# Optimization experiments

Hardware: AMD Instinct MI355X
Metric: run time of the kernel (lower is better)

The kernel has to match this reference:

```python
import jax, jax.numpy as jnp
import numpy as np

B, U, C, M = 4096, 1024, 5000, 20

def setup_inputs() -> dict:
    key = jax.random.key(0)
    ks = jax.random.split(key, 9)
    inputs = jax.random.randint(ks[0], (B, 1), 0, C).astype(jnp.int32)
    states = 0.1 * jax.random.normal(ks[1], (B, U + 2), dtype=jnp.float32)
    bias_z = jnp.zeros((U,), jnp.float32)
    recurrent_kernel = 0.02 * jax.random.normal(ks[2], (U, 4 * U), dtype=jnp.float32)
    kernel_c = 0.02 * jax.random.normal(ks[3], (C, 4 * U), dtype=jnp.float32)
    bias = jnp.zeros((3 * U,), jnp.float32)
    kernel_d = 0.1 * jax.random.normal(ks[4], (2, 4 * U), dtype=jnp.float32)
    Wgmm_part1 = 0.05 * jax.random.normal(ks[5], (U, 3 * M), dtype=jnp.float32)
    bgmm_part1 = jnp.zeros((3 * M,), jnp.float32)
    return {"inputs": inputs, "states": states, "bias_z": bias_z,
            "recurrent_kernel": recurrent_kernel, "kernel_c": kernel_c,
            "bias": bias, "kernel_d": kernel_d,
            "Wgmm_part1": Wgmm_part1, "bgmm_part1": bgmm_part1}

def exp_safe(x):
    return jnp.clip(jnp.exp(x), 1e-10, 1e10)

def reference(inputs, states, bias_z, recurrent_kernel, kernel_c, bias,
              kernel_d, Wgmm_part1, bgmm_part1):
    u = bias_z.shape[0]
    h_tm1 = states[:, :-2]          # [B, U]
    _d = states[:, -2:]             # [B, 2]
    ch = inputs[:, 0].astype(jnp.int32)
    # one_hot(ch) @ kernel_c is just a row gather
    pre = kernel_c[ch] + _d @ kernel_d              # [B, 4U]
    # z and r gates share the left operand -> fuse into one matmul
    zr = (h_tm1 @ recurrent_kernel[:, :2 * u] + pre[:, :2 * u]
          + jnp.concatenate([bias_z, bias[:u]]))
    z = jax.nn.sigmoid(zr[:, :u])
    r = jax.nn.sigmoid(zr[:, u:])
    hh = jnp.tanh((r * h_tm1) @ recurrent_kernel[:, 2 * u:3 * u]
                  + pre[:, 2 * u:3 * u] + bias[u:2 * u])
    h = z * h_tm1 + (1.0 - z) * hh
    o = jnp.tanh(h @ recurrent_kernel[:, 3 * u:]
                 + pre[:, 3 * u:] + bias[2 * u:])
    gmm = o @ Wgmm_part1 + bgmm_part1               # [B, 3M]
    _pi, mux, muy = jnp.split(gmm, 3, axis=-1)
    e = exp_safe(_pi)
    pi = e / jnp.sum(e, axis=-1, keepdims=True)
    x_pred = jnp.sum(pi * mux, axis=-1, keepdims=True)
    y_pred = jnp.sum(pi * muy, axis=-1, keepdims=True)
    out = jnp.concatenate([o, pi, mux, muy, x_pred, y_pred], axis=-1)
    new_state = jnp.concatenate([h, x_pred, y_pred], axis=-1)
    return out, new_state
```

## Files before the change

kernel.cpp:

```cpp
#include <hip/hip_runtime.h>

typedef __attribute__((ext_vector_type(8))) short     bf16x8;
typedef __attribute__((ext_vector_type(4))) float     f32x4;
typedef __attribute__((ext_vector_type(2))) float     f32x2;
typedef __attribute__((ext_vector_type(4))) unsigned short u16x4;

#define NB 4096
#define NU 1024
#define OUT_STRIDE 1086
#define NS_STRIDE 1026
#define NS_BASE (4096*1086)

__device__ __forceinline__ unsigned short f2bf(float x) {
  unsigned int u = __float_as_uint(x);
  unsigned int r = (u + 0x7FFFu + ((u >> 16) & 1u)) >> 16;
  return (unsigned short)r;
}
__device__ __forceinline__ float sigmoidf(float x) { return 1.f / (1.f + expf(-x)); }

__device__ __forceinline__ void gld_lds16(const void* g, void* l) {
  __builtin_amdgcn_global_load_lds((const __attribute__((address_space(1))) void*)g,
                                   (__attribute__((address_space(3))) void*)l, 16, 0, 0);
}

__global__ __launch_bounds__(256)
void transposeR(const float* __restrict__ R, unsigned short* __restrict__ Bt) {
  __shared__ float t[64][65];
  const int tx = threadIdx.x & 63, ty = threadIdx.x >> 6;
  const int j0 = blockIdx.x * 64, k0 = blockIdx.y * 64;
#pragma unroll
  for (int i = 0; i < 64; i += 4)
    t[ty + i][tx] = R[(size_t)(k0 + ty + i) * 4096 + j0 + tx];
  __syncthreads();
#pragma unroll
  for (int i = 0; i < 64; i += 4) {
    const int j = ty + i;
    Bt[(size_t)(j0 + j) * 1024 + k0 + tx] = f2bf(t[tx][j]);
  }
}

__global__ __launch_bounds__(256)
void convertH(const float* __restrict__ states, unsigned short* __restrict__ hb) {
  const int idx = blockIdx.x * 256 + threadIdx.x;
  const int b = idx >> 8, u = (idx & 255) * 4;
  const float* sp = states + (size_t)b * 1026 + u;
  f32x2 v0 = *(const f32x2*)sp, v1 = *(const f32x2*)(sp + 2);
  u16x4 w;
  w[0] = f2bf(v0[0]); w[1] = f2bf(v0[1]); w[2] = f2bf(v1[0]); w[3] = f2bf(v1[1]);
  *(u16x4*)&hb[(size_t)b * 1024 + u] = w;
}

template<int EPI>
__global__ __launch_bounds__(256)
void gemm_k(const unsigned short* __restrict__ A,
            const unsigned short* __restrict__ Bt,
            float* __restrict__ C, int ldc,
            const int* __restrict__ chv,
            const float* __restrict__ states,
            const float* __restrict__ kc, int colbase,
            const float* __restrict__ kd,
            const float* __restrict__ bias, int biasoff,
            const float* __restrict__ zbuf,
            float* __restrict__ out2,
            unsigned short* __restrict__ hb2) {
  __shared__ unsigned short Al[128 * 32];
  __shared__ unsigned short Bl[128 * 32];
  __shared__ int   chs[128];
  __shared__ float d0s[128], d1s[128];

  const int tid = threadIdx.x;
  const int lane = tid & 63;
  const int wave = tid >> 6;
  const int wr = wave >> 1, wc = wave & 1;
  const int m0 = blockIdx.y * 128;
  const int n0 = blockIdx.x * 128;

  if (EPI != 0 && tid < 128) {
    const int r = m0 + tid;
    chs[tid] = chv[r];
    d0s[tid] = states[(size_t)r * 1026 + 1024];
    d1s[tid] = states[(size_t)r * 1026 + 1025];
  }

  f32x4 acc[4][4] = {};

  const int c0 = tid, c1 = tid + 256;
  const int ar0 = c0 >> 2, ak0 = (c0 & 3) * 8;
  const int ar1 = c1 >> 2, ak1 = (c1 & 3) * 8;
  const unsigned short* Ag = A + (size_t)m0 * 1024;
  const unsigned short* Bg = Bt + (size_t)n0 * 1024;

  for (int k0 = 0; k0 < 1024; k0 += 32) {
    __syncthreads();
    gld_lds16(Ag + (size_t)ar0 * 1024 + k0 + ak0, &Al[c0 * 8]);
    gld_lds16(Ag + (size_t)ar1 * 1024 + k0 + ak1, &Al[c1 * 8]);
    gld_lds16(Bg + (size_t)ar0 * 1024 + k0 + ak0, &Bl[c0 * 8]);
    gld_lds16(Bg + (size_t)ar1 * 1024 + k0 + ak1, &Bl[c1 * 8]);
    __syncthreads();
    bf16x8 af[4], bfr[4];
    const int arow = lane & 15, kg = (lane >> 4) * 8;
#pragma unroll
    for (int mi = 0; mi < 4; ++mi)
      af[mi] = *(const bf16x8*)&Al[(wr * 64 + mi * 16 + arow) * 32 + kg];
#pragma unroll
    for (int ni = 0; ni < 4; ++ni)
      bfr[ni] = *(const bf16x8*)&Bl[(wc * 64 + ni * 16 + arow) * 32 + kg];
#pragma unroll
    for (int mi = 0; mi < 4; ++mi)
#pragma unroll
      for (int ni = 0; ni < 4; ++ni)
        acc[mi][ni] = __builtin_amdgcn_mfma_f32_16x16x32_bf16(af[mi], bfr[ni], acc[mi][ni], 0, 0, 0);
  }

#pragma unroll
  for (int mi = 0; mi < 4; ++mi) {
#pragma unroll
    for (int r = 0; r < 4; ++r) {
      const int lrow = wr * 64 + mi * 16 + (lane >> 4) * 4 + r;
      const int grow = m0 + lrow;
      if (EPI == 0) {
#pragma unroll
        for (int ni = 0; ni < 4; ++ni) {
          const int gcol = n0 + wc * 64 + ni * 16 + (lane & 15);
          C[(size_t)grow * ldc + gcol] = acc[mi][ni][r];
        }
      } else {
        const int ch = chs[lrow];
        const float d0 = d0s[lrow], d1 = d1s[lrow];
        const float* kcrow = kc + (size_t)ch * 4096 + colbase;
#pragma unroll
        for (int ni = 0; ni < 4; ++ni) {
          const int gcol = n0 + wc * 64 + ni * 16 + (lane & 15);
          float v = acc[mi][ni][r] + kcrow[gcol]
                  + d0 * kd[colbase + gcol] + d1 * kd[4096 + colbase + gcol]
                  + bias[biasoff + gcol];
          if (EPI == 2) {
            const float hh = tanhf(v);
            const float z = zbuf[(size_t)grow * 1024 + gcol];
            const float htm = states[(size_t)grow * 1026 + gcol];
            const float h = z * htm + (1.f - z) * hh;
            out2[(size_t)grow * NS_STRIDE + gcol] = h;
            hb2[(size_t)grow * 1024 + gcol] = f2bf(h);
          } else {
            out2[(size_t)grow * OUT_STRIDE + gcol] = tanhf(v);
          }
        }
      }
    }
  }
}

__global__ __launch_bounds__(256)
void epi1_kernel(const float* __restrict__ zr,
                 const int* __restrict__ chv,
                 const float* __restrict__ states,
                 const float* __restrict__ kc,
                 const float* __restrict__ kd,
                 const float* __restrict__ bias_z,
                 const float* __restrict__ bias,
                 float* __restrict__ zbuf,
                 unsigned short* __restrict__ rh) {
  const int idx = blockIdx.x * 256 + threadIdx.x;
  const int b = idx >> 8, u = (idx & 255) * 4;
  const int ch = chv[b];
  const float* srow = states + (size_t)b * 1026;
  const float d0 = srow[1024], d1 = srow[1025];
  f32x4 az = *(const f32x4*)&zr[(size_t)b * 2048 + u];
  f32x4 ar = *(const f32x4*)&zr[(size_t)b * 2048 + 1024 + u];
  const float* kcrow = kc + (size_t)ch * 4096;
  f32x4 kz = *(const f32x4*)&kcrow[u];
  f32x4 kr = *(const f32x4*)&kcrow[1024 + u];
  f32x4 kd0z = *(const f32x4*)&kd[u];
  f32x4 kd1z = *(const f32x4*)&kd[4096 + u];
  f32x4 kd0r = *(const f32x4*)&kd[1024 + u];
  f32x4 kd1r = *(const f32x4*)&kd[4096 + 1024 + u];
  f32x4 bz = *(const f32x4*)&bias_z[u];
  f32x4 br = *(const f32x4*)&bias[u];
  f32x2 h01 = *(const f32x2*)&srow[u];
  f32x2 h23 = *(const f32x2*)&srow[u + 2];
  float hv[4] = {h01[0], h01[1], h23[0], h23[1]};
  f32x4 zout;
  u16x4 rhv;
#pragma unroll
  for (int i = 0; i < 4; ++i) {
    const float zi = sigmoidf(az[i] + kz[i] + d0 * kd0z[i] + d1 * kd1z[i] + bz[i]);
    const float ri = sigmoidf(ar[i] + kr[i] + d0 * kd0r[i] + d1 * kd1r[i] + br[i]);
    zout[i] = zi;
    rhv[i] = f2bf(ri * hv[i]);
  }
  *(f32x4*)&zbuf[(size_t)b * 1024 + u] = zout;
  *(u16x4*)&rh[(size_t)b * 1024 + u] = rhv;
}

__global__ __launch_bounds__(512)
void gmm_kernel(const float* __restrict__ obuf,
                const float* __restrict__ Wg,
                const float* __restrict__ bg,
                float* __restrict__ outp,
                float* __restrict__ ns) {
  __shared__ float Wl[128 * 60 + 16];
  __shared__ float ol[8 * 1024];
  const int tid = threadIdx.x;
  const int lane = tid & 63;
  const int wave = tid >> 6;
  const int row0 = blockIdx.x * 8;

  for (int i = tid; i < 4096; i += 512) {
    const int rr = i >> 9, c2 = (i & 511) * 2;
    *(f32x2*)&ol[rr * 1024 + c2] = *(const f32x2*)&obuf[(size_t)(row0 + rr) * OUT_STRIDE + c2];
  }

  float g = 0.f;
  for (int kc0 = 0; kc0 < 1024; kc0 += 128) {
    __syncthreads();
    for (int i = tid; i < 1920; i += 512)
      *(f32x4*)&Wl[i * 4] = *(const f32x4*)&Wg[kc0 * 60 + i * 4];
    __syncthreads();
    const float* orow = &ol[wave * 1024 + kc0];
#pragma unroll 8
    for (int k = 0; k < 128; ++k)
      g = fmaf(orow[k], Wl[k * 60 + lane], g);
  }
  if (lane < 60) g += bg[lane];

  float e = 0.f;
  if (lane < 20) e = fminf(fmaxf(expf(g), 1e-10f), 1e10f);
  float s = e;
#pragma unroll
  for (int m = 1; m < 32; m <<= 1) s += __shfl_xor(s, m, 64);
  const float pi = (lane < 20) ? e / s : 0.f;
  const int src1 = (lane < 20) ? lane + 20 : lane;
  const int src2 = (lane < 20) ? lane + 40 : lane;
  const float mux = __shfl(g, src1, 64);
  const float muy = __shfl(g, src2, 64);
  float px = pi * mux, py = pi * muy;
#pragma unroll
  for (int m = 1; m < 32; m <<= 1) { px += __shfl_xor(px, m, 64); py += __shfl_xor(py, m, 64); }

  const int row = row0 + wave;
  float* orow = outp + (size_t)row * OUT_STRIDE;
  if (lane < 20) orow[1024 + lane] = pi;
  else if (lane < 60) orow[1024 + lane] = g;
  if (lane == 0) {
    orow[1084] = px;
    orow[1085] = py;
    ns[(size_t)row * NS_STRIDE + 1024] = px;
    ns[(size_t)row * NS_STRIDE + 1025] = py;
  }
}

extern "C" void kernel_launch(void* const* d_in, const int* in_sizes, int n_in,
                              void* d_out, int out_size, void* d_ws, size_t ws_size,
                              hipStream_t stream) {
  const int*   chv     = (const int*)d_in[0];
  const float* states  = (const float*)d_in[1];
  const float* bias_z  = (const float*)d_in[2];
  const float* R       = (const float*)d_in[3];
  const float* kc      = (const float*)d_in[4];
  const float* bias    = (const float*)d_in[5];
  const float* kd      = (const float*)d_in[6];
  const float* Wg      = (const float*)d_in[7];
  const float* bg      = (const float*)d_in[8];
  float* out = (float*)d_out;

  char* ws = (char*)d_ws;
  unsigned short* RbT = (unsigned short*)ws;
  unsigned short* hb  = (unsigned short*)(ws + 8388608);
  float*          zr  = (float*)(ws + 16777216);
  float*          zbuf= (float*)(ws + 50331648);
  unsigned short* rh  = hb;
  unsigned short* hb2 = (unsigned short*)zr;

  transposeR<<<dim3(64, 16), 256, 0, stream>>>(R, RbT);
  convertH<<<4096, 256, 0, stream>>>(states, hb);

  gemm_k<0><<<dim3(16, 32), 256, 0, stream>>>(hb, RbT, zr, 2048,
      nullptr, nullptr, nullptr, 0, nullptr, nullptr, 0, nullptr, nullptr, nullptr);

  epi1_kernel<<<4096, 256, 0, stream>>>(zr, chv, states, kc, kd, bias_z, bias, zbuf, rh);

  gemm_k<2><<<dim3(8, 32), 256, 0, stream>>>(rh, RbT + (size_t)2048 * 1024, nullptr, 0,
      chv, states, kc, 2048, kd, bias, 1024, zbuf, out + NS_BASE, hb2);

  gemm_k<3><<<dim3(8, 32), 256, 0, stream>>>(hb2, RbT + (size_t)3072 * 1024, nullptr, 0,
      chv, states, kc, 3072, kd, bias, 2048, nullptr, out, nullptr);

  gmm_kernel<<<512, 512, 0, stream>>>(out, Wg, bg, out, out + NS_BASE);
}
```

Baseline: 343.9 us.

## Fuse z/r gate epilogue into GEMM, double-buffer LDS, swizzle block order

Merges the z/r GEMM and its sigmoid epilogue into a single kernel that computes the matching z and r column tiles together. This removes the fp32 zr intermediate round-trip and one kernel launch. All GEMMs move to 128x64 tiles with double-buffered LDS prefetch and a swizzled 1D block mapping meant to improve L2 reuse. r*h now uses the bf16-rounded h instead of fp32 states, a small change in precision.

```diff
diff --git a/kernel.cpp b/kernel.cpp
--- a/kernel.cpp
+++ b/kernel.cpp
@@ -5,8 +5,6 @@
 typedef __attribute__((ext_vector_type(2))) float     f32x2;
 typedef __attribute__((ext_vector_type(4))) unsigned short u16x4;
 
-#define NB 4096
-#define NU 1024
 #define OUT_STRIDE 1086
 #define NS_STRIDE 1026
 #define NS_BASE (4096*1086)
@@ -16,11 +14,21 @@
   unsigned int r = (u + 0x7FFFu + ((u >> 16) & 1u)) >> 16;
   return (unsigned short)r;
 }
+__device__ __forceinline__ float bf2f(unsigned short u) {
+  union { unsigned int i; float f; } v; v.i = ((unsigned int)u) << 16; return v.f;
+}
 __device__ __forceinline__ float sigmoidf(float x) { return 1.f / (1.f + expf(-x)); }
 
 __device__ __forceinline__ void gld_lds16(const void* g, void* l) {
   __builtin_amdgcn_global_load_lds((const __attribute__((address_space(1))) void*)g,
                                    (__attribute__((address_space(3))) void*)l, 16, 0, 0);
+}
+
+__device__ __forceinline__ void decode_block(int bid, int& m0, int& n0) {
+  const int swz = (bid & 7) * 64 + (bid >> 3);
+  const int chunk = swz >> 6, l = swz & 63;
+  m0 = ((chunk & 3) * 8 + (l >> 3)) * 128;
+  n0 = ((chunk >> 2) * 8 + (l & 7)) * 64;
 }
 
 __global__ __launch_bounds__(256)
@@ -50,11 +58,106 @@
   *(u16x4*)&hb[(size_t)b * 1024 + u] = w;
 }
 
+__global__ __launch_bounds__(256)
+void gemm_zr(const unsigned short* __restrict__ A,
+             const unsigned short* __restrict__ Bt,
+             const int* __restrict__ chv,
+             const float* __restrict__ states,
+             const float* __restrict__ kc,
+             const float* __restrict__ kd,
+             const float* __restrict__ bias_z,
+             const float* __restrict__ bias,
+             float* __restrict__ zbuf,
+             unsigned short* __restrict__ rh) {
+  __shared__ unsigned short Al[2][128 * 32];
+  __shared__ unsigned short Bzl[2][64 * 32];
+  __shared__ unsigned short Brl[2][64 * 32];
+  __shared__ int   chs[128];
+  __shared__ float d0s[128], d1s[128];
+
+  const int tid = threadIdx.x, lane = tid & 63, wave = tid >> 6;
+  int m0, n0;
+  decode_block(blockIdx.x, m0, n0);
+
+  if (tid < 128) {
+    const int r = m0 + tid;
+    chs[tid] = chv[r];
+    d0s[tid] = states[(size_t)r * 1026 + 1024];
+    d1s[tid] = states[(size_t)r * 1026 + 1025];
+  }
+
+  const unsigned short* Ag  = A  + (size_t)m0 * 1024;
+  const unsigned short* Bzg = Bt + (size_t)n0 * 1024;
+  const unsigned short* Brg = Bt + (size_t)(1024 + n0) * 1024;
+
+  const int c1 = tid + 256;
+  const int ar0 = tid >> 2, ak0 = (tid & 3) * 8;
+  const int ar1 = c1 >> 2,  ak1 = (c1 & 3) * 8;
+
+  f32x4 accz[2][4] = {}, accr[2][4] = {};
+
+#define STAGE_ZR(b, kk)                                                        \
+  gld_lds16(Ag  + (size_t)ar0 * 1024 + (kk) + ak0, &Al[b][tid * 8]);           \
+  gld_lds16(Ag  + (size_t)ar1 * 1024 + (kk) + ak1, &Al[b][c1 * 8]);            \
+  gld_lds16(Bzg + (size_t)ar0 * 1024 + (kk) + ak0, &Bzl[b][tid * 8]);          \
+  gld_lds16(Brg + (size_t)ar0 * 1024 + (kk) + ak0, &Brl[b][tid * 8]);
+
+  STAGE_ZR(0, 0);
+  __syncthreads();
+
+  const int arow = lane & 15, kg = (lane >> 4) * 8;
+  for (int t = 0; t < 32; ++t) {
+    const int cb = t & 1;
+    if (t < 31) { STAGE_ZR(cb ^ 1, (t + 1) * 32); }
+    bf16x8 af[2], bzf[4], brf[4];
+#pragma unroll
+    for (int mi = 0; mi < 2; ++mi)
+      af[mi] = *(const bf16x8*)&Al[cb][(wave * 32 + mi * 16 + arow) * 32 + kg];
+#pragma unroll
+    for (int ni = 0; ni < 4; ++ni) {
+      bzf[ni] = *(const bf16x8*)&Bzl[cb][(ni * 16 + arow) * 32 + kg];
+      brf[ni] = *(const bf16x8*)&Brl[cb][(ni * 16 + arow) * 32 + kg];
+    }
+#pragma unroll
+    for (int mi = 0; mi < 2; ++mi)
+#pragma unroll
+      for (int ni = 0; ni < 4; ++ni) {
+        accz[mi][ni] = __builtin_amdgcn_mfma_f32_16x16x32_bf16(af[mi], bzf[ni], accz[mi][ni], 0, 0, 0);
+        accr[mi][ni] = __builtin_amdgcn_mfma_f32_16x16x32_bf16(af[mi], brf[ni], accr[mi][ni], 0, 0, 0);
+      }
+    if (t < 31) __syncthreads();
+  }
+#undef STAGE_ZR
+
+#pragma unroll
+  for (int mi = 0; mi < 2; ++mi) {
+#pragma unroll
+    for (int r = 0; r < 4; ++r) {
+      const int lrow = wave * 32 + mi * 16 + (lane >> 4) * 4 + r;
+      const int grow = m0 + lrow;
+      const int ch = chs[lrow];
+      const float d0 = d0s[lrow], d1 = d1s[lrow];
+      const float* kcrow = kc + (size_t)ch * 4096;
+#pragma unroll
+      for (int ni = 0; ni < 4; ++ni) {
+        const int jc = n0 + ni * 16 + (lane & 15);
+        const float vz = accz[mi][ni][r] + kcrow[jc]
+                       + d0 * kd[jc] + d1 * kd[4096 + jc] + bias_z[jc];
+        const float vr = accr[mi][ni][r] + kcrow[1024 + jc]
+                       + d0 * kd[1024 + jc] + d1 * kd[4096 + 1024 + jc] + bias[jc];
+        const float z = sigmoidf(vz);
+        const float rr = sigmoidf(vr);
+        zbuf[(size_t)grow * 1024 + jc] = z;
+        rh[(size_t)grow * 1024 + jc] = f2bf(rr * bf2f(A[(size_t)grow * 1024 + jc]));
+      }
+    }
+  }
+}
+
 template<int EPI>
 __global__ __launch_bounds__(256)
 void gemm_k(const unsigned short* __restrict__ A,
             const unsigned short* __restrict__ Bt,
-            float* __restrict__ C, int ldc,
             const int* __restrict__ chv,
             const float* __restrict__ states,
             const float* __restrict__ kc, int colbase,
@@ -63,133 +166,87 @@
             const float* __restrict__ zbuf,
             float* __restrict__ out2,
             unsigned short* __restrict__ hb2) {
-  __shared__ unsigned short Al[128 * 32];
-  __shared__ unsigned short Bl[128 * 32];
+  __shared__ unsigned short Al[2][128 * 32];
+  __shared__ unsigned short Bl[2][64 * 32];
   __shared__ int   chs[128];
   __shared__ float d0s[128], d1s[128];
 
-  const int tid = threadIdx.x;
-  const int lane = tid & 63;
-  const int wave = tid >> 6;
-  const int wr = wave >> 1, wc = wave & 1;
-  const int m0 = blockIdx.y * 128;
-  const int n0 = blockIdx.x * 128;
-
-  if (EPI != 0 && tid < 128) {
+  const int tid = threadIdx.x, lane = tid & 63, wave = tid >> 6;
+  int m0, n0;
+  decode_block(blockIdx.x, m0, n0);
+
+  if (tid < 128) {
     const int r = m0 + tid;
     chs[tid] = chv[r];
     d0s[tid] = states[(size_t)r * 1026 + 1024];
     d1s[tid] = states[(size_t)r * 1026 + 1025];
   }
 
-  f32x4 acc[4][4] = {};
-
-  const int c0 = tid, c1 = tid + 256;
-  const int ar0 = c0 >> 2, ak0 = (c0 & 3) * 8;
-  const int ar1 = c1 >> 2, ak1 = (c1 & 3) * 8;
-  const unsigned short* Ag = A + (size_t)m0 * 1024;
+  const unsigned short* Ag = A  + (size_t)m0 * 1024;
   const unsigned short* Bg = Bt + (size_t)n0 * 1024;
 
-  for (int k0 = 0; k0 < 1024; k0 += 32) {
-    __syncthreads();
-    gld_lds16(Ag + (size_t)ar0 * 1024 + k0 + ak0, &Al[c0 * 8]);
-    gld_lds16(Ag + (size_t)ar1 * 1024 + k0 + ak1, &Al[c1 * 8]);
-    gld_lds16(Bg + (size_t)ar0 * 1024 + k0 + ak0, &Bl[c0 * 8]);
-    gld_lds16(Bg + (size_t)ar1 * 1024 + k0 + ak1, &Bl[c1 * 8]);
-    __syncthreads();
-    bf16x8 af[4], bfr[4];
-    const int arow = lane & 15, kg = (lane >> 4) * 8;
-#pragma unroll
-    for (int mi = 0; mi < 4; ++mi)
-      af[mi] = *(const bf16x8*)&Al[(wr * 64 + mi * 16 + arow) * 32 + kg];
+  const int c1 = tid + 256;
+  const int ar0 = tid >> 2, ak0 = (tid & 3) * 8;
+  const int ar1 = c1 >> 2,  ak1 = (c1 & 3) * 8;
+
+  f32x4 acc[2][4] = {};
+
+#define STAGE_K(b, kk)                                                         \
+  gld_lds16(Ag + (size_t)ar0 * 1024 + (kk) + ak0, &Al[b][tid * 8]);            \
+  gld_lds16(Ag + (size_t)ar1 * 1024 + (kk) + ak1, &Al[b][c1 * 8]);             \
+  gld_lds16(Bg + (size_t)ar0 * 1024 + (kk) + ak0, &Bl[b][tid * 8]);
+
+  STAGE_K(0, 0);
+  __syncthreads();
+
+  const int arow = lane & 15, kg = (lane >> 4) * 8;
+  for (int t = 0; t < 32; ++t) {
+    const int cb = t & 1;
+    if (t < 31) { STAGE_K(cb ^ 1, (t + 1) * 32); }
+    bf16x8 af[2], bf[4];
+#pragma unroll
+    for (int mi = 0; mi < 2; ++mi)
+      af[mi] = *(const bf16x8*)&Al[cb][(wave * 32 + mi * 16 + arow) * 32 + kg];
 #pragma unroll
     for (int ni = 0; ni < 4; ++ni)
-      bfr[ni] = *(const bf16x8*)&Bl[(wc * 64 + ni * 16 + arow) * 32 + kg];
-#pragma unroll
-    for (int mi = 0; mi < 4; ++mi)
+      bf[ni] = *(const bf16x8*)&Bl[cb][(ni * 16 + arow) * 32 + kg];
+#pragma unroll
+    for (int mi = 0; mi < 2; ++mi)
 #pragma unroll
       for (int ni = 0; ni < 4; ++ni)
-        acc[mi][ni] = __builtin_amdgcn_mfma_f32_16x16x32_bf16(af[mi], bfr[ni], acc[mi][ni], 0, 0, 0);
-  }
-
-#pragma unroll
-  for (int mi = 0; mi < 4; ++mi) {
+        acc[mi][ni] = __builtin_amdgcn_mfma_f32_16x16x32_bf16(af[mi], bf[ni], acc[mi][ni], 0, 0, 0);
+    if (t < 31) __syncthreads();
+  }
+#undef STAGE_K
+
+#pragma unroll
+  for (int mi = 0; mi < 2; ++mi) {
 #pragma unroll
     for (int r = 0; r < 4; ++r) {
-      const int lrow = wr * 64 + mi * 16 + (lane >> 4) * 4 + r;
+      const int lrow = wave * 32 + mi * 16 + (lane >> 4) * 4 + r;
       const int grow = m0 + lrow;
-      if (EPI == 0) {
-#pragma unroll
-        for (int ni = 0; ni < 4; ++ni) {
-          const int gcol = n0 + wc * 64 + ni * 16 + (lane & 15);
-          C[(size_t)grow * ldc + gcol] = acc[mi][ni][r];
-        }
-      } else {
-        const int ch = chs[lrow];
-        const float d0 = d0s[lrow], d1 = d1s[lrow];
-        const float* kcrow = kc + (size_t)ch * 4096 + colbase;
-#pragma unroll
-        for (int ni = 0; ni < 4; ++ni) {
-          const int gcol = n0 + wc * 64 + ni * 16 + (lane & 15);
-          float v = acc[mi][ni][r] + kcrow[gcol]
-                  + d0 * kd[colbase + gcol] + d1 * kd[4096 + colbase + gcol]
-                  + bias[biasoff + gcol];
-          if (EPI == 2) {
-            const float hh = tanhf(v);
-            const float z = zbuf[(size_t)grow * 1024 + gcol];
-            const float htm = states[(size_t)grow * 1026 + gcol];
-            const float h = z * htm + (1.f - z) * hh;
-            out2[(size_t)grow * NS_STRIDE + gcol] = h;
-            hb2[(size_t)grow * 1024 + gcol] = f2bf(h);
-          } else {
-            out2[(size_t)grow * OUT_STRIDE + gcol] = tanhf(v);
-          }
+      const int ch = chs[lrow];
+      const float d0 = d0s[lrow], d1 = d1s[lrow];
+      const float* kcrow = kc + (size_t)ch * 4096 + colbase;
+#pragma unroll
+      for (int ni = 0; ni < 4; ++ni) {
+        const int gcol = n0 + ni * 16 + (lane & 15);
+        float v = acc[mi][ni][r] + kcrow[gcol]
+                + d0 * kd[colbase + gcol] + d1 * kd[4096 + colbase + gcol]
+                + bias[biasoff + gcol];
+        if (EPI == 2) {
+          const float hh = tanhf(v);
+          const float z = zbuf[(size_t)grow * 1024 + gcol];
+          const float htm = states[(size_t)grow * 1026 + gcol];
+          const float h = z * htm + (1.f - z) * hh;
+          out2[(size_t)grow * NS_STRIDE + gcol] = h;
+          hb2[(size_t)grow * 1024 + gcol] = f2bf(h);
+        } else {
+          out2[(size_t)grow * OUT_STRIDE + gcol] = tanhf(v);
         }
       }
     }
   }
-}
-
-__global__ __launch_bounds__(256)
-void epi1_kernel(const float* __restrict__ zr,
-                 const int* __restrict__ chv,
-                 const float* __restrict__ states,
-                 const float* __restrict__ kc,
-                 const float* __restrict__ kd,
-                 const float* __restrict__ bias_z,
-                 const float* __restrict__ bias,
-                 float* __restrict__ zbuf,
-                 unsigned short* __restrict__ rh) {
-  const int idx = blockIdx.x * 256 + threadIdx.x;
-  const int b = idx >> 8, u = (idx & 255) * 4;
-  const int ch = chv[b];
-  const float* srow = states + (size_t)b * 1026;
-  const float d0 = srow[1024], d1 = srow[1025];
-  f32x4 az = *(const f32x4*)&zr[(size_t)b * 2048 + u];
-  f32x4 ar = *(const f32x4*)&zr[(size_t)b * 2048 + 1024 + u];
-  const float* kcrow = kc + (size_t)ch * 4096;
-  f32x4 kz = *(const f32x4*)&kcrow[u];
-  f32x4 kr = *(const f32x4*)&kcrow[1024 + u];
-  f32x4 kd0z = *(const f32x4*)&kd[u];
-  f32x4 kd1z = *(const f32x4*)&kd[4096 + u];
-  f32x4 kd0r = *(const f32x4*)&kd[1024 + u];
-  f32x4 kd1r = *(const f32x4*)&kd[4096 + 1024 + u];
-  f32x4 bz = *(const f32x4*)&bias_z[u];
-  f32x4 br = *(const f32x4*)&bias[u];
-  f32x2 h01 = *(const f32x2*)&srow[u];
-  f32x2 h23 = *(const f32x2*)&srow[u + 2];
-  float hv[4] = {h01[0], h01[1], h23[0], h23[1]};
-  f32x4 zout;
-  u16x4 rhv;
-#pragma unroll
-  for (int i = 0; i < 4; ++i) {
-    const float zi = sigmoidf(az[i] + kz[i] + d0 * kd0z[i] + d1 * kd1z[i] + bz[i]);
-    const float ri = sigmoidf(ar[i] + kr[i] + d0 * kd0r[i] + d1 * kd1r[i] + br[i]);
-    zout[i] = zi;
-    rhv[i] = f2bf(ri * hv[i]);
-  }
-  *(f32x4*)&zbuf[(size_t)b * 1024 + u] = zout;
-  *(u16x4*)&rh[(size_t)b * 1024 + u] = rhv;
 }
 
 __global__ __launch_bounds__(512)
@@ -252,37 +309,33 @@
 extern "C" void kernel_launch(void* const* d_in, const int* in_sizes, int n_in,
                               void* d_out, int out_size, void* d_ws, size_t ws_size,
                               hipStream_t stream) {
-  const int*   chv     = (const int*)d_in[0];
-  const float* states  = (const float*)d_in[1];
-  const float* bias_z  = (const float*)d_in[2];
-  const float* R       = (const float*)d_in[3];
-  const float* kc      = (const float*)d_in[4];
-  const float* bias    = (const float*)d_in[5];
-  const float* kd      = (const float*)d_in[6];
-  const float* Wg      = (const float*)d_in[7];
-  const float* bg      = (const float*)d_in[8];
+  const int*   chv    = (const int*)d_in[0];
+  const float* states = (const float*)d_in[1];
+  const float* bias_z = (const float*)d_in[2];
+  const float* R      = (const float*)d_in[3];
+  const float* kc     = (const float*)d_in[4];
+  const float* bias   = (const float*)d_in[5];
+  const float* kd     = (const float*)d_in[6];
+  const float* Wg     = (const float*)d_in[7];
+  const float* bg     = (const float*)d_in[8];
   float* out = (float*)d_out;
 
   char* ws = (char*)d_ws;
-  unsigned short* RbT = (unsigned short*)ws;
-  unsigned short* hb  = (unsigned short*)(ws + 8388608);
-  float*          zr  = (float*)(ws + 16777216);
-  float*          zbuf= (float*)(ws + 50331648);
-  unsigned short* rh  = hb;
-  unsigned short* hb2 = (unsigned short*)zr;
+  unsigned short* RbT  = (unsigned short*)ws;
+  unsigned short* hb   = (unsigned short*)(ws + 8388608);
+  unsigned short* rh   = (unsigned short*)(ws + 16777216);
+  unsigned short* hb2  = (unsigned short*)(ws + 25165824);
+  float*          zbuf = (float*)(ws + 33554432);
 
   transposeR<<<dim3(64, 16), 256, 0, stream>>>(R, RbT);
   convertH<<<4096, 256, 0, stream>>>(states, hb);
 
-  gemm_k<0><<<dim3(16, 32), 256, 0, stream>>>(hb, RbT, zr, 2048,
-      nullptr, nullptr, nullptr, 0, nullptr, nullptr, 0, nullptr, nullptr, nullptr);
-
-  epi1_kernel<<<4096, 256, 0, stream>>>(zr, chv, states, kc, kd, bias_z, bias, zbuf, rh);
-
-  gemm_k<2><<<dim3(8, 32), 256, 0, stream>>>(rh, RbT + (size_t)2048 * 1024, nullptr, 0,
+  gemm_zr<<<512, 256, 0, stream>>>(hb, RbT, chv, states, kc, kd, bias_z, bias, zbuf, rh);
+
+  gemm_k<2><<<512, 256, 0, stream>>>(rh, RbT + (size_t)2048 * 1024,
       chv, states, kc, 2048, kd, bias, 1024, zbuf, out + NS_BASE, hb2);
 
-  gemm_k<3><<<dim3(8, 32), 256, 0, stream>>>(hb2, RbT + (size_t)3072 * 1024, nullptr, 0,
+  gemm_k<3><<<512, 256, 0, stream>>>(hb2, RbT + (size_t)3072 * 1024,
       chv, states, kc, 3072, kd, bias, 2048, nullptr, out, nullptr);
 
   gmm_kernel<<<512, 512, 0, stream>>>(out, Wg, bg, out, out + NS_BASE);
```

Result: no change. 339.8 us (-1.2%).

## Fuse GRU gate GEMMs and epilogues into one row-resident mega kernel

Applied to the files above, without the earlier changes.

Replaces convertH, three tiled GEMMs and the separate z/r epilogue kernel with a single kernel. Each 512-thread block owns 16 batch rows, keeps h, r*h and z in LDS as bf16 with a swizzled layout, and streams the transposed recurrent weights through a small LDS ring buffer. This removes global round trips for the zr, zbuf and intermediate bf16 activations and several launches. In exchange each block re-reads the whole weight matrix (256 blocks × 8 MB bf16), relying on L2/MALL. It uses only a 16×16 MFMA tile per wave with little reuse, and storing z in bf16 reduces precision.

```diff
diff --git a/kernel.cpp b/kernel.cpp
--- a/kernel.cpp
+++ b/kernel.cpp
@@ -3,24 +3,33 @@
 typedef __attribute__((ext_vector_type(8))) short     bf16x8;
 typedef __attribute__((ext_vector_type(4))) float     f32x4;
 typedef __attribute__((ext_vector_type(2))) float     f32x2;
-typedef __attribute__((ext_vector_type(4))) unsigned short u16x4;
-
-#define NB 4096
-#define NU 1024
+
 #define OUT_STRIDE 1086
 #define NS_STRIDE 1026
 #define NS_BASE (4096*1086)
+
+#define HA_OFF 0
+#define RH_OFF 32768
+#define ZB_OFF 65536
+#define B_OFF  98304
 
 __device__ __forceinline__ unsigned short f2bf(float x) {
   unsigned int u = __float_as_uint(x);
   unsigned int r = (u + 0x7FFFu + ((u >> 16) & 1u)) >> 16;
   return (unsigned short)r;
 }
+__device__ __forceinline__ float bf2f(unsigned short u) {
+  union { unsigned int i; float f; } v; v.i = ((unsigned int)u) << 16; return v.f;
+}
 __device__ __forceinline__ float sigmoidf(float x) { return 1.f / (1.f + expf(-x)); }
 
 __device__ __forceinline__ void gld_lds16(const void* g, void* l) {
   __builtin_amdgcn_global_load_lds((const __attribute__((address_space(1))) void*)g,
                                    (__attribute__((address_space(3))) void*)l, 16, 0, 0);
+}
+
+__device__ __forceinline__ int swz(int row, int koff) {
+  return row * 2048 + (koff ^ ((row & 7) << 4));
 }
 
 __global__ __launch_bounds__(256)
@@ -39,157 +48,155 @@
   }
 }
 
-__global__ __launch_bounds__(256)
-void convertH(const float* __restrict__ states, unsigned short* __restrict__ hb) {
-  const int idx = blockIdx.x * 256 + threadIdx.x;
-  const int b = idx >> 8, u = (idx & 255) * 4;
-  const float* sp = states + (size_t)b * 1026 + u;
-  f32x2 v0 = *(const f32x2*)sp, v1 = *(const f32x2*)(sp + 2);
-  u16x4 w;
-  w[0] = f2bf(v0[0]); w[1] = f2bf(v0[1]); w[2] = f2bf(v1[0]); w[3] = f2bf(v1[1]);
-  *(u16x4*)&hb[(size_t)b * 1024 + u] = w;
-}
-
-template<int EPI>
-__global__ __launch_bounds__(256)
-void gemm_k(const unsigned short* __restrict__ A,
-            const unsigned short* __restrict__ Bt,
-            float* __restrict__ C, int ldc,
-            const int* __restrict__ chv,
-            const float* __restrict__ states,
-            const float* __restrict__ kc, int colbase,
-            const float* __restrict__ kd,
-            const float* __restrict__ bias, int biasoff,
-            const float* __restrict__ zbuf,
-            float* __restrict__ out2,
-            unsigned short* __restrict__ hb2) {
-  __shared__ unsigned short Al[128 * 32];
-  __shared__ unsigned short Bl[128 * 32];
-  __shared__ int   chs[128];
-  __shared__ float d0s[128], d1s[128];
-
-  const int tid = threadIdx.x;
-  const int lane = tid & 63;
-  const int wave = tid >> 6;
-  const int wr = wave >> 1, wc = wave & 1;
-  const int m0 = blockIdx.y * 128;
-  const int n0 = blockIdx.x * 128;
-
-  if (EPI != 0 && tid < 128) {
-    const int r = m0 + tid;
-    chs[tid] = chv[r];
-    d0s[tid] = states[(size_t)r * 1026 + 1024];
-    d1s[tid] = states[(size_t)r * 1026 + 1025];
-  }
-
-  f32x4 acc[4][4] = {};
-
-  const int c0 = tid, c1 = tid + 256;
-  const int ar0 = c0 >> 2, ak0 = (c0 & 3) * 8;
-  const int ar1 = c1 >> 2, ak1 = (c1 & 3) * 8;
-  const unsigned short* Ag = A + (size_t)m0 * 1024;
-  const unsigned short* Bg = Bt + (size_t)n0 * 1024;
-
-  for (int k0 = 0; k0 < 1024; k0 += 32) {
-    __syncthreads();
-    gld_lds16(Ag + (size_t)ar0 * 1024 + k0 + ak0, &Al[c0 * 8]);
-    gld_lds16(Ag + (size_t)ar1 * 1024 + k0 + ak1, &Al[c1 * 8]);
-    gld_lds16(Bg + (size_t)ar0 * 1024 + k0 + ak0, &Bl[c0 * 8]);
-    gld_lds16(Bg + (size_t)ar1 * 1024 + k0 + ak1, &Bl[c1 * 8]);
-    __syncthreads();
-    bf16x8 af[4], bfr[4];
-    const int arow = lane & 15, kg = (lane >> 4) * 8;
-#pragma unroll
-    for (int mi = 0; mi < 4; ++mi)
-      af[mi] = *(const bf16x8*)&Al[(wr * 64 + mi * 16 + arow) * 32 + kg];
-#pragma unroll
-    for (int ni = 0; ni < 4; ++ni)
-      bfr[ni] = *(const bf16x8*)&Bl[(wc * 64 + ni * 16 + arow) * 32 + kg];
-#pragma unroll
-    for (int mi = 0; mi < 4; ++mi)
-#pragma unroll
-      for (int ni = 0; ni < 4; ++ni)
-        acc[mi][ni] = __builtin_amdgcn_mfma_f32_16x16x32_bf16(af[mi], bfr[ni], acc[mi][ni], 0, 0, 0);
-  }
-
-#pragma unroll
-  for (int mi = 0; mi < 4; ++mi) {
-#pragma unroll
-    for (int r = 0; r < 4; ++r) {
-      const int lrow = wr * 64 + mi * 16 + (lane >> 4) * 4 + r;
-      const int grow = m0 + lrow;
-      if (EPI == 0) {
-#pragma unroll
-        for (int ni = 0; ni < 4; ++ni) {
-          const int gcol = n0 + wc * 64 + ni * 16 + (lane & 15);
-          C[(size_t)grow * ldc + gcol] = acc[mi][ni][r];
+__global__ __launch_bounds__(512, 2)
+void mega(const unsigned short* __restrict__ Bt,
+          const int* __restrict__ chv,
+          const float* __restrict__ states,
+          const float* __restrict__ kcm,
+          const float* __restrict__ kd,
+          const float* __restrict__ bias_z,
+          const float* __restrict__ bias,
+          float* __restrict__ out,
+          float* __restrict__ ns) {
+  __shared__ __align__(16) char lds[147456];
+  const int tid = threadIdx.x, lane = tid & 63, wave = tid >> 6;
+  const int fr = lane & 15, fq = lane >> 4;
+  const int r0 = blockIdx.x * 16;
+
+  int chr_[4]; float d0r[4], d1r[4];
+#pragma unroll
+  for (int i = 0; i < 4; ++i) {
+    const int grow = r0 + fq * 4 + i;
+    chr_[i] = chv[grow];
+    d0r[i] = states[(size_t)grow * 1026 + 1024];
+    d1r[i] = states[(size_t)grow * 1026 + 1025];
+  }
+
+  const size_t soff = (size_t)(tid >> 2) * 1024 + (size_t)(tid & 3) * 8;
+
+  auto stage1 = [&](int g) {
+    const int tile = g >> 5, k0 = (g & 31) * 32;
+    const size_t src = (size_t)(tile * 128) * 1024 + k0 + soff;
+    gld_lds16(Bt + src,                       lds + B_OFF + ((2 * g)     % 6) * 8192 + tid * 16);
+    gld_lds16(Bt + (size_t)1024 * 1024 + src, lds + B_OFF + ((2 * g + 1) % 6) * 8192 + tid * 16);
+  };
+  stage1(0); stage1(1);
+
+  {
+    const int tr = tid >> 5, cb = (tid & 31) * 32;
+    const float* sp = states + (size_t)(r0 + tr) * 1026 + cb;
+#pragma unroll
+    for (int j = 0; j < 4; ++j) {
+      f32x4 a = *(const f32x4*)(sp + j * 8);
+      f32x4 b = *(const f32x4*)(sp + j * 8 + 4);
+      union { unsigned short us[8]; bf16x8 v; } u;
+      u.us[0] = f2bf(a[0]); u.us[1] = f2bf(a[1]); u.us[2] = f2bf(a[2]); u.us[3] = f2bf(a[3]);
+      u.us[4] = f2bf(b[0]); u.us[5] = f2bf(b[1]); u.us[6] = f2bf(b[2]); u.us[7] = f2bf(b[3]);
+      *(bf16x8*)(lds + HA_OFF + swz(tr, cb * 2 + j * 16)) = u.v;
+    }
+  }
+  __syncthreads();
+
+  const int bro = (wave * 16 + fr) * 64 + fq * 16;
+  const f32x4 zero4 = {0.f, 0.f, 0.f, 0.f};
+
+  {
+    f32x4 accz = zero4, accr = zero4;
+    for (int g = 0; g < 256; ++g) {
+      const int k0 = (g & 31) * 32;
+      if (g < 255) asm volatile("s_waitcnt vmcnt(2)" ::: "memory");
+      else         asm volatile("s_waitcnt vmcnt(0)" ::: "memory");
+      __builtin_amdgcn_s_barrier();
+      bf16x8 af  = *(const bf16x8*)(lds + HA_OFF + swz(fr, k0 * 2 + fq * 16));
+      bf16x8 bzf = *(const bf16x8*)(lds + B_OFF + ((2 * g)     % 6) * 8192 + bro);
+      bf16x8 brf = *(const bf16x8*)(lds + B_OFF + ((2 * g + 1) % 6) * 8192 + bro);
+      if (g + 2 < 256) stage1(g + 2);
+      accz = __builtin_amdgcn_mfma_f32_16x16x32_bf16(af, bzf, accz, 0, 0, 0);
+      accr = __builtin_amdgcn_mfma_f32_16x16x32_bf16(af, brf, accr, 0, 0, 0);
+      if ((g & 31) == 31) {
+        const int c = (g >> 5) * 128 + wave * 16 + fr;
+#pragma unroll
+        for (int i = 0; i < 4; ++i) {
+          const int row = fq * 4 + i, grow = r0 + row;
+          const float* kcr = kcm + (size_t)chr_[i] * 4096;
+          const float vz = accz[i] + kcr[c]        + d0r[i] * kd[c]        + d1r[i] * kd[4096 + c]        + bias_z[c];
+          const float vr = accr[i] + kcr[1024 + c] + d0r[i] * kd[1024 + c] + d1r[i] * kd[4096 + 1024 + c] + bias[c];
+          const float z  = sigmoidf(vz);
+          const float rr = sigmoidf(vr);
+          const float htm = states[(size_t)grow * 1026 + c];
+          *(unsigned short*)(lds + ZB_OFF + swz(row, c * 2)) = f2bf(z);
+          *(unsigned short*)(lds + RH_OFF + swz(row, c * 2)) = f2bf(rr * htm);
         }
-      } else {
-        const int ch = chs[lrow];
-        const float d0 = d0s[lrow], d1 = d1s[lrow];
-        const float* kcrow = kc + (size_t)ch * 4096 + colbase;
-#pragma unroll
-        for (int ni = 0; ni < 4; ++ni) {
-          const int gcol = n0 + wc * 64 + ni * 16 + (lane & 15);
-          float v = acc[mi][ni][r] + kcrow[gcol]
-                  + d0 * kd[colbase + gcol] + d1 * kd[4096 + colbase + gcol]
-                  + bias[biasoff + gcol];
-          if (EPI == 2) {
-            const float hh = tanhf(v);
-            const float z = zbuf[(size_t)grow * 1024 + gcol];
-            const float htm = states[(size_t)grow * 1026 + gcol];
-            const float h = z * htm + (1.f - z) * hh;
-            out2[(size_t)grow * NS_STRIDE + gcol] = h;
-            hb2[(size_t)grow * 1024 + gcol] = f2bf(h);
-          } else {
-            out2[(size_t)grow * OUT_STRIDE + gcol] = tanhf(v);
-          }
+        accz = zero4; accr = zero4;
+      }
+    }
+  }
+  __syncthreads();
+
+  auto stageN = [&](int g, const unsigned short* Bp) {
+    const int tile = g >> 5, k0 = (g & 31) * 32;
+    gld_lds16(Bp + (size_t)(tile * 128) * 1024 + k0 + soff,
+              lds + B_OFF + (g % 3) * 8192 + tid * 16);
+  };
+  {
+    const unsigned short* Bp = Bt + (size_t)2048 * 1024;
+    stageN(0, Bp); stageN(1, Bp);
+    f32x4 acc = zero4;
+    for (int g = 0; g < 256; ++g) {
+      const int k0 = (g & 31) * 32;
+      if (g < 255) asm volatile("s_waitcnt vmcnt(1)" ::: "memory");
+      else         asm volatile("s_waitcnt vmcnt(0)" ::: "memory");
+      __builtin_amdgcn_s_barrier();
+      bf16x8 af = *(const bf16x8*)(lds + RH_OFF + swz(fr, k0 * 2 + fq * 16));
+      bf16x8 bf_ = *(const bf16x8*)(lds + B_OFF + (g % 3) * 8192 + bro);
+      if (g + 2 < 256) stageN(g + 2, Bp);
+      acc = __builtin_amdgcn_mfma_f32_16x16x32_bf16(af, bf_, acc, 0, 0, 0);
+      if ((g & 31) == 31) {
+        const int c = (g >> 5) * 128 + wave * 16 + fr;
+#pragma unroll
+        for (int i = 0; i < 4; ++i) {
+          const int row = fq * 4 + i, grow = r0 + row;
+          const float* kcr = kcm + (size_t)chr_[i] * 4096;
+          const float v = acc[i] + kcr[2048 + c] + d0r[i] * kd[2048 + c] + d1r[i] * kd[4096 + 2048 + c] + bias[1024 + c];
+          const float hh = tanhf(v);
+          const float z  = bf2f(*(const unsigned short*)(lds + ZB_OFF + swz(row, c * 2)));
+          const float htm = states[(size_t)grow * 1026 + c];
+          const float h = z * htm + (1.f - z) * hh;
+          ns[(size_t)grow * NS_STRIDE + c] = h;
+          *(unsigned short*)(lds + HA_OFF + swz(row, c * 2)) = f2bf(h);
         }
+        acc = zero4;
       }
     }
   }
-}
-
-__global__ __launch_bounds__(256)
-void epi1_kernel(const float* __restrict__ zr,
-                 const int* __restrict__ chv,
-                 const float* __restrict__ states,
-                 const float* __restrict__ kc,
-                 const float* __restrict__ kd,
-                 const float* __restrict__ bias_z,
-                 const float* __restrict__ bias,
-                 float* __restrict__ zbuf,
-                 unsigned short* __restrict__ rh) {
-  const int idx = blockIdx.x * 256 + threadIdx.x;
-  const int b = idx >> 8, u = (idx & 255) * 4;
-  const int ch = chv[b];
-  const float* srow = states + (size_t)b * 1026;
-  const float d0 = srow[1024], d1 = srow[1025];
-  f32x4 az = *(const f32x4*)&zr[(size_t)b * 2048 + u];
-  f32x4 ar = *(const f32x4*)&zr[(size_t)b * 2048 + 1024 + u];
-  const float* kcrow = kc + (size_t)ch * 4096;
-  f32x4 kz = *(const f32x4*)&kcrow[u];
-  f32x4 kr = *(const f32x4*)&kcrow[1024 + u];
-  f32x4 kd0z = *(const f32x4*)&kd[u];
-  f32x4 kd1z = *(const f32x4*)&kd[4096 + u];
-  f32x4 kd0r = *(const f32x4*)&kd[1024 + u];
-  f32x4 kd1r = *(const f32x4*)&kd[4096 + 1024 + u];
-  f32x4 bz = *(const f32x4*)&bias_z[u];
-  f32x4 br = *(const f32x4*)&bias[u];
-  f32x2 h01 = *(const f32x2*)&srow[u];
-  f32x2 h23 = *(const f32x2*)&srow[u + 2];
-  float hv[4] = {h01[0], h01[1], h23[0], h23[1]};
-  f32x4 zout;
-  u16x4 rhv;
-#pragma unroll
-  for (int i = 0; i < 4; ++i) {
-    const float zi = sigmoidf(az[i] + kz[i] + d0 * kd0z[i] + d1 * kd1z[i] + bz[i]);
-    const float ri = sigmoidf(ar[i] + kr[i] + d0 * kd0r[i] + d1 * kd1r[i] + br[i]);
-    zout[i] = zi;
-    rhv[i] = f2bf(ri * hv[i]);
-  }
-  *(f32x4*)&zbuf[(size_t)b * 1024 + u] = zout;
-  *(u16x4*)&rh[(size_t)b * 1024 + u] = rhv;
+  __syncthreads();
+
+  {
+    const unsigned short* Bp = Bt + (size_t)3072 * 1024;
+    stageN(0, Bp); stageN(1, Bp);
+    f32x4 acc = zero4;
+    for (int g = 0; g < 256; ++g) {
+      const int k0 = (g & 31) * 32;
+      if (g < 255) asm volatile("s_waitcnt vmcnt(1)" ::: "memory");
+      else         asm volatile("s_waitcnt vmcnt(0)" ::: "memory");
+      __builtin_amdgcn_s_barrier();
+      bf16x8 af = *(const bf16x8*)(lds + HA_OFF + swz(fr, k0 * 2 + fq * 16));
+      bf16x8 bf_ = *(const bf16x8*)(lds + B_OFF + (g % 3) * 8192 + bro);
+      if (g + 2 < 256) stageN(g + 2, Bp);
+      acc = __builtin_amdgcn_mfma_f32_16x16x32_bf16(af, bf_, acc, 0, 0, 0);
+      if ((g & 31) == 31) {
+        const int c = (g >> 5) * 128 + wave * 16 + fr;
+#pragma unroll
+        for (int i = 0; i < 4; ++i) {
+          const int row = fq * 4 + i, grow = r0 + row;
+          const float* kcr = kcm + (size_t)chr_[i] * 4096;
+          const float v = acc[i] + kcr[3072 + c] + d0r[i] * kd[3072 + c] + d1r[i] * kd[4096 + 3072 + c] + bias[2048 + c];
+          out[(size_t)grow * OUT_STRIDE + c] = tanhf(v);
+        }
+        acc = zero4;
+      }
+    }
+  }
 }
 
 __global__ __launch_bounds__(512)
@@ -252,38 +259,23 @@
 extern "C" void kernel_launch(void* const* d_in, const int* in_sizes, int n_in,
                               void* d_out, int out_size, void* d_ws, size_t ws_size,
                               hipStream_t stream) {
-  const int*   chv     = (const int*)d_in[0];
-  const float* states  = (const float*)d_in[1];
-  const float* bias_z  = (const float*)d_in[2];
-  const float* R       = (const float*)d_in[3];
-  const float* kc      = (const float*)d_in[4];
-  const float* bias    = (const float*)d_in[5];
-  const float* kd      = (const float*)d_in[6];
-  const float* Wg      = (const float*)d_in[7];
-  const float* bg      = (const float*)d_in[8];
+  const int*   chv    = (const int*)d_in[0];
+  const float* states = (const float*)d_in[1];
+  const float* bias_z = (const float*)d_in[2];
+  const float* R      = (const float*)d_in[3];
+  const float* kc     = (const float*)d_in[4];
+  const float* bias   = (const float*)d_in[5];
+  const float* kd     = (const float*)d_in[6];
+  const float* Wg     = (const float*)d_in[7];
+  const float* bg     = (const float*)d_in[8];
   float* out = (float*)d_out;
 
-  char* ws = (char*)d_ws;
-  unsigned short* RbT = (unsigned short*)ws;
-  unsigned short* hb  = (unsigned short*)(ws + 8388608);
-  float*          zr  = (float*)(ws + 16777216);
-  float*          zbuf= (float*)(ws + 50331648);
-  unsigned short* rh  = hb;
-  unsigned short* hb2 = (unsigned short*)zr;
+  unsigned short* RbT = (unsigned short*)d_ws;
 
   transposeR<<<dim3(64, 16), 256, 0, stream>>>(R, RbT);
-  convertH<<<4096, 256, 0, stream>>>(states, hb);
-
-  gemm_k<0><<<dim3(16, 32), 256, 0, stream>>>(hb, RbT, zr, 2048,
-      nullptr, nullptr, nullptr, 0, nullptr, nullptr, 0, nullptr, nullptr, nullptr);
-
-  epi1_kernel<<<4096, 256, 0, stream>>>(zr, chv, states, kc, kd, bias_z, bias, zbuf, rh);
-
-  gemm_k<2><<<dim3(8, 32), 256, 0, stream>>>(rh, RbT + (size_t)2048 * 1024, nullptr, 0,
-      chv, states, kc, 2048, kd, bias, 1024, zbuf, out + NS_BASE, hb2);
-
-  gemm_k<3><<<dim3(8, 32), 256, 0, stream>>>(hb2, RbT + (size_t)3072 * 1024, nullptr, 0,
-      chv, states, kc, 3072, kd, bias, 2048, nullptr, out, nullptr);
+
+  mega<<<256, 512, 0, stream>>>(RbT, chv, states, kc, kd, bias_z, bias,
+                                out, out + NS_BASE);
 
   gmm_kernel<<<512, 512, 0, stream>>>(out, Wg, bg, out, out + NS_BASE);
 }
```

Result: slower. 409.9 us (+19.2%).
